# Performance work log

Measured on AMD Instinct MI355X. Metric: run time of the kernel, lower is better.

Reference implementation:

```python
import jax, jax.numpy as jnp
import numpy as np

D = 1024
H = 16
HD = D // H
EPS = 1e-6


def setup_inputs() -> dict:
    key = jax.random.key(0)
    ks = jax.random.split(key, 10)
    s = 1.0 / np.sqrt(D)
    inp = {
        "x": jax.random.normal(ks[0], (2, 2048, D), dtype=jnp.float32),
        "Wq": jax.random.uniform(ks[1], (D, D), jnp.float32, -s, s),
        "bq": jax.random.uniform(ks[2], (D,), jnp.float32, -s, s),
        "Wk": jax.random.uniform(ks[3], (D, D), jnp.float32, -s, s),
        "bk": jax.random.uniform(ks[4], (D,), jnp.float32, -s, s),
        "Wv": jax.random.uniform(ks[5], (D, D), jnp.float32, -s, s),
        "bv": jax.random.uniform(ks[6], (D,), jnp.float32, -s, s),
        "Wo": jax.random.uniform(ks[7], (D, D), jnp.float32, -s, s),
        "bo": jax.random.uniform(ks[8], (D,), jnp.float32, -s, s),
        "gamma": jnp.ones((D,), jnp.float32),
        "beta": jnp.zeros((D,), jnp.float32),
    }
    return inp


def _mha(x, Wq, bq, Wk, bk, Wv, bv, Wo, bo, gamma, beta):
    B, S, _ = x.shape
    # Linear projections (torch Linear: x @ W.T + b), split heads -> [B,H,S,hd]
    q = (x @ Wq.T + bq).reshape(B, S, H, HD).transpose(0, 2, 1, 3)
    k = (x @ Wk.T + bk).reshape(B, S, H, HD).transpose(0, 2, 1, 3)
    v = (x @ Wv.T + bv).reshape(B, S, H, HD).transpose(0, 2, 1, 3)
    scores = jnp.einsum("bhqd,bhkd->bhqk", q, k) / jnp.sqrt(jnp.float32(HD))
    attn = jax.nn.softmax(scores, axis=-1)
    ctx = jnp.einsum("bhqk,bhkd->bhqd", attn, v)
    ctx = ctx.transpose(0, 2, 1, 3).reshape(B, S, D)
    out = ctx @ Wo.T + bo  # dropout p=0.0 -> identity
    res = x + out
    mu = jnp.mean(res, axis=-1, keepdims=True)
    var = jnp.mean(jnp.square(res - mu), axis=-1, keepdims=True)
    return (res - mu) / jnp.sqrt(var + EPS) * gamma + beta


def reference(x, Wq, bq, Wk, bk, Wv, bv, Wo, bo, gamma, beta):
    return _mha(x, Wq, bq, Wk, bk, Wv, bv, Wo, bo, gamma, beta)
```

## Files before the change

kernel.cpp:

```cpp
#include <hip/hip_runtime.h>
#include <hip/hip_bf16.h>
#include <math.h>

#define D_MODEL 1024
#define NH 16
#define HDIM 64
#define BB 2
#define SS 2048
#define MTOK (BB*SS)

typedef __hip_bfloat16 bf16;
typedef short s8v __attribute__((ext_vector_type(8)));
typedef float f4v __attribute__((ext_vector_type(4)));
typedef float f16v __attribute__((ext_vector_type(16)));

__device__ __forceinline__ float bf2f(bf16 x) { return __bfloat162float(x); }
__device__ __forceinline__ bf16 f2bf(float x) { return __float2bfloat16(x); }

typedef const __attribute__((address_space(1))) unsigned int* gas_u32;
typedef __attribute__((address_space(3))) unsigned int* las_u32;
#define ASYNC16(gp, lp) __builtin_amdgcn_global_load_lds((gas_u32)(gp), (las_u32)(lp), 16, 0, 0)

#define QSCALE 0.18033688f

__device__ __forceinline__ unsigned int pack_bf16(float a, float b) {
    unsigned int ua = __builtin_bit_cast(unsigned int, a);
    unsigned int ub = __builtin_bit_cast(unsigned int, b);
    return ((ua + 0x8000u) >> 16) | ((ub + 0x8000u) & 0xffff0000u);
}

__global__ __launch_bounds__(256)
void cvt_kernel(const float* __restrict__ x,  const float* __restrict__ wq,
                const float* __restrict__ wk, const float* __restrict__ wv,
                const float* __restrict__ wo, bf16* __restrict__ dst)
{
    const size_t e = ((size_t)blockIdx.x * 256 + threadIdx.x) * 4;
    const size_t M1 = (size_t)1 << 20;
    const float* src; size_t off;
    if      (e < 4 * M1) { src = x;  off = e;          }
    else if (e < 5 * M1) { src = wq; off = e - 4 * M1; }
    else if (e < 6 * M1) { src = wk; off = e - 5 * M1; }
    else if (e < 7 * M1) { src = wv; off = e - 6 * M1; }
    else                 { src = wo; off = e - 7 * M1; }
    const float4 v = *(const float4*)&src[off];
    bf16 h[4] = { f2bf(v.x), f2bf(v.y), f2bf(v.z), f2bf(v.w) };
    *(uint2*)&dst[e] = *(const uint2*)h;
}

__global__ __launch_bounds__(256, 2)
void gemm_qkv(const bf16* __restrict__ X,
              const bf16* __restrict__ Wq, const float* __restrict__ bq,
              const bf16* __restrict__ Wk, const float* __restrict__ bk,
              const bf16* __restrict__ Wv, const float* __restrict__ bv,
              bf16* __restrict__ q_ws, bf16* __restrict__ k_ws, bf16* __restrict__ v_ws)
{
    const int mat = blockIdx.z;
    const bf16*  W    = (mat == 0) ? Wq : ((mat == 1) ? Wk : Wv);
    const float* bias = (mat == 0) ? bq : ((mat == 1) ? bk : bv);

    const int t = threadIdx.x;
    const int lane = t & 63, wave = t >> 6;
    const int wrow = wave >> 1, wcol = wave & 1;
    const int quad = lane >> 4, l15 = lane & 15;

    const bf16 *Ap, *Bp; int m0, n0;
    if (mat < 2) { Ap = X; Bp = W; m0 = blockIdx.y * 128; n0 = blockIdx.x * 128; }
    else         { Ap = W; Bp = X; m0 = blockIdx.x * 128; n0 = blockIdx.y * 128; }

    __shared__ __align__(16) bf16 As[128 * 64];
    __shared__ __align__(16) bf16 Bs[128 * 64];

    f4v acc[4][4];
#pragma unroll
    for (int i = 0; i < 4; i++)
#pragma unroll
        for (int j = 0; j < 4; j++) acc[i][j] = (f4v){0.f, 0.f, 0.f, 0.f};

    for (int kk = 0; kk < D_MODEL; kk += 64) {
#pragma unroll
        for (int p = 0; p < 4; p++) {
            const int c = p * 256 + t;
            const int row = c >> 3, j = c & 7;
            ASYNC16(&Ap[(size_t)(m0 + row) * D_MODEL + kk + (j ^ (row & 7)) * 8], &As[c * 8]);
        }
#pragma unroll
        for (int p = 0; p < 4; p++) {
            const int c = p * 256 + t;
            const int row = c >> 3, j = c & 7;
            ASYNC16(&Bp[(size_t)(n0 + row) * D_MODEL + kk + (j ^ (row & 7)) * 8], &Bs[c * 8]);
        }
        __syncthreads();

#pragma unroll
        for (int ks = 0; ks < 2; ks++) {
            s8v af[4], bf_[4];
#pragma unroll
            for (int i = 0; i < 4; i++) {
                const int row = wrow * 64 + i * 16 + l15;
                const int g = (ks * 4 + quad) ^ (row & 7);
                af[i] = *(const s8v*)&As[row * 64 + g * 8];
            }
#pragma unroll
            for (int j = 0; j < 4; j++) {
                const int row = wcol * 64 + j * 16 + l15;
                const int g = (ks * 4 + quad) ^ (row & 7);
                bf_[j] = *(const s8v*)&Bs[row * 64 + g * 8];
            }
#pragma unroll
            for (int i = 0; i < 4; i++)
#pragma unroll
                for (int j = 0; j < 4; j++)
                    acc[i][j] = __builtin_amdgcn_mfma_f32_16x16x32_bf16(af[i], bf_[j], acc[i][j], 0, 0, 0);
        }
        __syncthreads();
    }

    if (mat == 2) {
#pragma unroll
        for (int i = 0; i < 4; i++) {
#pragma unroll
            for (int r = 0; r < 4; r++) {
                const int f = m0 + wrow * 64 + i * 16 + quad * 4 + r;
                const float bv_ = bias[f];
#pragma unroll
                for (int j = 0; j < 4; j++) {
                    const int tok = n0 + wcol * 64 + j * 16 + l15;
                    const int b = tok >> 11, s = tok & 2047;
                    v_ws[((size_t)(b * D_MODEL + f)) * SS + s] = f2bf(acc[i][j][r] + bv_);
                }
            }
        }
    } else {
        bf16* dst = (mat == 0) ? q_ws : k_ws;
        const float scale = (mat == 0) ? QSCALE : 1.0f;
#pragma unroll
        for (int j = 0; j < 4; j++) {
            const int col = n0 + wcol * 64 + j * 16 + l15;
            const float bv_ = bias[col];
            const int h = col >> 6, hd = col & 63;
#pragma unroll
            for (int i = 0; i < 4; i++) {
#pragma unroll
                for (int r = 0; r < 4; r++) {
                    const int row = m0 + wrow * 64 + i * 16 + quad * 4 + r;
                    const int b = row >> 11, s = row & 2047;
                    const float v = (acc[i][j][r] + bv_) * scale;
                    dst[(((size_t)(b * NH + h)) * SS + s) * HDIM + hd] = f2bf(v);
                }
            }
        }
    }
}

__global__ __launch_bounds__(256, 2)
void attn_kernel(const bf16* __restrict__ Q, const bf16* __restrict__ K,
                 const bf16* __restrict__ VtG, bf16* __restrict__ ctx)
{
    const int s_ = blockIdx.x;
    const int lb = (s_ & 7) * 64 + (s_ >> 3);
    const int bh = lb >> 4;
    const int q0 = (lb & 15) * 128;
    const bf16* Qp = Q   + (size_t)bh * SS * HDIM;
    const bf16* Kp = K   + (size_t)bh * SS * HDIM;
    const bf16* Vp = VtG + (size_t)bh * HDIM * SS;

    __shared__ __align__(16) bf16 Qs[128 * 64];
    __shared__ __align__(16) bf16 Ks[2][128 * 64];
    __shared__ __align__(16) bf16 Vt[2][64 * 128];

    const int t = threadIdx.x;
    const int lane = t & 63, wave = t >> 6;
    const int l31 = lane & 31, L5 = lane >> 5;
    const int qb = wave * 32;

    const int vrbase = t >> 4;
    const int vcol = (t & 15) * 8;
    uint4 vv[4];
#pragma unroll
    for (int p = 0; p < 4; p++)
        vv[p] = *(const uint4*)&Vp[(size_t)(p * 16 + vrbase) * SS + vcol];
#pragma unroll
    for (int p = 0; p < 4; p++) {
        const int c = p * 256 + t;
        const int row = c >> 3, j = c & 7;
        ASYNC16(&Kp[(size_t)row * HDIM + (j ^ (row & 7)) * 8], &Ks[0][c * 8]);
    }
#pragma unroll
    for (int p = 0; p < 4; p++) {
        const int c = p * 256 + t;
        const int row = c >> 3, g = (c & 7) ^ (row & 7);
        *(uint4*)&Qs[row * 64 + g * 8] = *(const uint4*)&Qp[(size_t)(q0 + row) * HDIM + (c & 7) * 8];
    }
    const int cA = vcol,     pA = (cA & ~12) | ((cA & 4) << 1) | ((cA & 8) >> 1);
    const int cB = vcol + 4, pB = (cB & ~12) | ((cB & 4) << 1) | ((cB & 8) >> 1);
    {
        union { uint4 u4; uint2 u2[2]; } uu;
#pragma unroll
        for (int p = 0; p < 4; p++) {
            const int vr = p * 16 + vrbase;
            uu.u4 = vv[p];
            *(uint2*)&Vt[0][vr * 128 + (((pA >> 3) ^ (vr & 15)) * 8) + (pA & 7)] = uu.u2[0];
            *(uint2*)&Vt[0][vr * 128 + (((pB >> 3) ^ (vr & 15)) * 8) + (pB & 7)] = uu.u2[1];
        }
    }
    __syncthreads();

    s8v qf[4];
#pragma unroll
    for (int kc = 0; kc < 4; kc++) {
        const int g = (kc * 2 + L5) ^ (l31 & 7);
        qf[kc] = *(const s8v*)&Qs[(qb + l31) * 64 + g * 8];
    }

    float l_own = 0.f;
    f16v o_acc[2];
#pragma unroll
    for (int i = 0; i < 16; i++) { o_acc[0][i] = 0.f; o_acc[1][i] = 0.f; }

    int cur = 0;
    for (int it = 0; it < SS / 128; ++it) {
        const bool have = (it < SS / 128 - 1);
        const int s0n = (it + 1) * 128;

        uint4 nv0, nv1, nv2, nv3;
        if (have) {
            nv0 = *(const uint4*)&Vp[(size_t)(0 * 16 + vrbase) * SS + s0n + vcol];
            nv1 = *(const uint4*)&Vp[(size_t)(1 * 16 + vrbase) * SS + s0n + vcol];
            nv2 = *(const uint4*)&Vp[(size_t)(2 * 16 + vrbase) * SS + s0n + vcol];
            nv3 = *(const uint4*)&Vp[(size_t)(3 * 16 + vrbase) * SS + s0n + vcol];
#pragma unroll
            for (int p = 0; p < 4; p++) {
                const int c = p * 256 + t;
                const int row = c >> 3, j = c & 7;
                ASYNC16(&Kp[(size_t)(s0n + row) * HDIM + (j ^ (row & 7)) * 8],
                        &Ks[cur ^ 1][c * 8]);
            }
        }

        const bf16* Ksc = &Ks[cur][0];
        const bf16* Vtc = &Vt[cur][0];
#pragma unroll
        for (int mt = 0; mt < 4; mt++) {
            f16v sc;
#pragma unroll
            for (int i = 0; i < 16; i++) sc[i] = 0.f;
            __builtin_amdgcn_s_setprio(1);
#pragma unroll
            for (int kc = 0; kc < 4; kc++) {
                const int g = (kc * 2 + L5) ^ (l31 & 7);
                const s8v kf = *(const s8v*)&Ksc[(mt * 32 + l31) * 64 + g * 8];
                sc = __builtin_amdgcn_mfma_f32_32x32x16_bf16(kf, qf[kc], sc, 0, 0, 0);
            }
            __builtin_amdgcn_s_setprio(0);
            float tps = 0.f;
#pragma unroll
            for (int i = 0; i < 16; i++) { sc[i] = __builtin_amdgcn_exp2f(sc[i]); tps += sc[i]; }
            l_own += tps;
            unsigned int pk[8];
#pragma unroll
            for (int i = 0; i < 8; i++) pk[i] = pack_bf16(sc[2 * i], sc[2 * i + 1]);
            __builtin_amdgcn_s_setprio(1);
#pragma unroll
            for (int c = 0; c < 2; c++) {
                const s8v pf = *(const s8v*)&pk[c * 4];
#pragma unroll
                for (int dt = 0; dt < 2; dt++) {
                    const int g = (mt * 4 + c * 2 + L5) ^ (l31 & 15);
                    const s8v vf = *(const s8v*)&Vtc[(dt * 32 + l31) * 128 + g * 8];
                    o_acc[dt] = __builtin_amdgcn_mfma_f32_32x32x16_bf16(pf, vf, o_acc[dt], 0, 0, 0);
                }
            }
            __builtin_amdgcn_s_setprio(0);
        }

        if (have) {
            bf16* VtN = &Vt[cur ^ 1][0];
            union { uint4 u4; uint2 u2[2]; } uu;
            const int vr0 = 0 * 16 + vrbase, vr1 = 1 * 16 + vrbase;
            const int vr2 = 2 * 16 + vrbase, vr3 = 3 * 16 + vrbase;
            uu.u4 = nv0;
            *(uint2*)&VtN[vr0 * 128 + (((pA >> 3) ^ (vr0 & 15)) * 8) + (pA & 7)] = uu.u2[0];
            *(uint2*)&VtN[vr0 * 128 + (((pB >> 3) ^ (vr0 & 15)) * 8) + (pB & 7)] = uu.u2[1];
            uu.u4 = nv1;
            *(uint2*)&VtN[vr1 * 128 + (((pA >> 3) ^ (vr1 & 15)) * 8) + (pA & 7)] = uu.u2[0];
            *(uint2*)&VtN[vr1 * 128 + (((pB >> 3) ^ (vr1 & 15)) * 8) + (pB & 7)] = uu.u2[1];
            uu.u4 = nv2;
            *(uint2*)&VtN[vr2 * 128 + (((pA >> 3) ^ (vr2 & 15)) * 8) + (pA & 7)] = uu.u2[0];
            *(uint2*)&VtN[vr2 * 128 + (((pB >> 3) ^ (vr2 & 15)) * 8) + (pB & 7)] = uu.u2[1];
            uu.u4 = nv3;
            *(uint2*)&VtN[vr3 * 128 + (((pA >> 3) ^ (vr3 & 15)) * 8) + (pA & 7)] = uu.u2[0];
            *(uint2*)&VtN[vr3 * 128 + (((pB >> 3) ^ (vr3 & 15)) * 8) + (pB & 7)] = uu.u2[1];
        }
        __syncthreads();
        cur ^= 1;
    }

    const float l_full = l_own + __shfl_xor(l_own, 32);
    const float linv = 1.0f / l_full;
    const int b = bh >> 4, h = bh & 15;
#pragma unroll
    for (int reg = 0; reg < 16; reg++) {
        const int R = (reg & 3) + 8 * (reg >> 2) + 4 * L5;
        const float lr = __shfl(linv, R);
        const int tok = q0 + qb + R;
        const size_t rb = ((size_t)(b * SS + tok)) * D_MODEL + h * 64;
        ctx[rb + l31]      = f2bf(o_acc[0][reg] * lr);
        ctx[rb + 32 + l31] = f2bf(o_acc[1][reg] * lr);
    }
}

__global__ __launch_bounds__(256, 2)
void gemm_oproj(const bf16* __restrict__ Ctx, const bf16* __restrict__ Wo,
                const float* __restrict__ bo, const float* __restrict__ X,
                float* __restrict__ res)
{
    const int m0 = blockIdx.y * 128, n0 = blockIdx.x * 128;
    const int t = threadIdx.x;
    const int lane = t & 63, wave = t >> 6;
    const int wrow = wave >> 1, wcol = wave & 1;
    const int quad = lane >> 4, l15 = lane & 15;

    __shared__ __align__(16) bf16 As[128 * 64];
    __shared__ __align__(16) bf16 Bs[128 * 64];

    f4v acc[4][4];
#pragma unroll
    for (int i = 0; i < 4; i++)
#pragma unroll
        for (int j = 0; j < 4; j++) acc[i][j] = (f4v){0.f, 0.f, 0.f, 0.f};

    for (int kk = 0; kk < D_MODEL; kk += 64) {
#pragma unroll
        for (int p = 0; p < 4; p++) {
            const int c = p * 256 + t;
            const int row = c >> 3, j = c & 7;
            ASYNC16(&Ctx[(size_t)(m0 + row) * D_MODEL + kk + (j ^ (row & 7)) * 8], &As[c * 8]);
        }
#pragma unroll
        for (int p = 0; p < 4; p++) {
            const int c = p * 256 + t;
            const int row = c >> 3, j = c & 7;
            ASYNC16(&Wo[(size_t)(n0 + row) * D_MODEL + kk + (j ^ (row & 7)) * 8], &Bs[c * 8]);
        }
        __syncthreads();

#pragma unroll
        for (int ks = 0; ks < 2; ks++) {
            s8v af[4], bf_[4];
#pragma unroll
            for (int i = 0; i < 4; i++) {
                const int row = wrow * 64 + i * 16 + l15;
                const int g = (ks * 4 + quad) ^ (row & 7);
                af[i] = *(const s8v*)&As[row * 64 + g * 8];
            }
#pragma unroll
            for (int j = 0; j < 4; j++) {
                const int row = wcol * 64 + j * 16 + l15;
                const int g = (ks * 4 + quad) ^ (row & 7);
                bf_[j] = *(const s8v*)&Bs[row * 64 + g * 8];
            }
#pragma unroll
            for (int i = 0; i < 4; i++)
#pragma unroll
                for (int j = 0; j < 4; j++)
                    acc[i][j] = __builtin_amdgcn_mfma_f32_16x16x32_bf16(af[i], bf_[j], acc[i][j], 0, 0, 0);
        }
        __syncthreads();
    }

#pragma unroll
    for (int j = 0; j < 4; j++) {
        const int col = n0 + wcol * 64 + j * 16 + l15;
        const float bv_ = bo[col];
#pragma unroll
        for (int i = 0; i < 4; i++) {
#pragma unroll
            for (int r = 0; r < 4; r++) {
                const int row = m0 + wrow * 64 + i * 16 + quad * 4 + r;
                const size_t idx = (size_t)row * D_MODEL + col;
                res[idx] = acc[i][j][r] + bv_ + X[idx];
            }
        }
    }
}

__global__ __launch_bounds__(256)
void ln_kernel(const float* __restrict__ res, const float* __restrict__ gamma,
               const float* __restrict__ beta, float* __restrict__ out)
{
    const int row = blockIdx.x;
    const int t = threadIdx.x;
    const float4 v = *(const float4*)&res[(size_t)row * D_MODEL + t * 4];

    float s = v.x + v.y + v.z + v.w;
    float sq = v.x * v.x + v.y * v.y + v.z * v.z + v.w * v.w;
#pragma unroll
    for (int m = 1; m < 64; m <<= 1) {
        s += __shfl_xor(s, m);
        sq += __shfl_xor(sq, m);
    }
    __shared__ float red[8];
    const int wave = t >> 6, lane = t & 63;
    if (lane == 0) { red[wave] = s; red[4 + wave] = sq; }
    __syncthreads();
    s = red[0] + red[1] + red[2] + red[3];
    sq = red[4] + red[5] + red[6] + red[7];
    const float mu = s * (1.0f / D_MODEL);
    const float var = sq * (1.0f / D_MODEL) - mu * mu;
    const float rstd = rsqrtf(var + 1e-6f);

    const float vv[4] = {v.x, v.y, v.z, v.w};
    float4 o;
    o.x = (vv[0] - mu) * rstd * gamma[t * 4 + 0] + beta[t * 4 + 0];
    o.y = (vv[1] - mu) * rstd * gamma[t * 4 + 1] + beta[t * 4 + 1];
    o.z = (vv[2] - mu) * rstd * gamma[t * 4 + 2] + beta[t * 4 + 2];
    o.w = (vv[3] - mu) * rstd * gamma[t * 4 + 3] + beta[t * 4 + 3];
    *(float4*)&out[(size_t)row * D_MODEL + t * 4] = o;
}

extern "C" void kernel_launch(void* const* d_in, const int* in_sizes, int n_in,
                              void* d_out, int out_size, void* d_ws, size_t ws_size,
                              hipStream_t stream) {
    const float* x     = (const float*)d_in[0];
    const float* Wq    = (const float*)d_in[1];
    const float* bq    = (const float*)d_in[2];
    const float* Wk    = (const float*)d_in[3];
    const float* bk    = (const float*)d_in[4];
    const float* Wv    = (const float*)d_in[5];
    const float* bv    = (const float*)d_in[6];
    const float* Wo    = (const float*)d_in[7];
    const float* bo    = (const float*)d_in[8];
    const float* gamma = (const float*)d_in[9];
    const float* beta  = (const float*)d_in[10];
    float* out = (float*)d_out;

    char* ws = (char*)d_ws;
    bf16* xb  = (bf16*)(ws);
    bf16* Wqb = (bf16*)(ws + ((size_t)8 << 20));
    bf16* Wkb = (bf16*)(ws + ((size_t)10 << 20));
    bf16* Wvb = (bf16*)(ws + ((size_t)12 << 20));
    bf16* Wob = (bf16*)(ws + ((size_t)14 << 20));
    bf16*  q_ws   = (bf16*)(ws + ((size_t)16 << 20));
    bf16*  k_ws   = (bf16*)(ws + ((size_t)24 << 20));
    bf16*  v_ws   = (bf16*)(ws + ((size_t)32 << 20));
    bf16*  ctx_ws = (bf16*)(ws + ((size_t)40 << 20));
    float* res_ws = (float*)(ws + ((size_t)16 << 20));

    cvt_kernel<<<8192, 256, 0, stream>>>(x, Wq, Wk, Wv, Wo, xb);
    gemm_qkv<<<dim3(8, 32, 3), 256, 0, stream>>>(xb, Wqb, bq, Wkb, bk, Wvb, bv, q_ws, k_ws, v_ws);
    attn_kernel<<<512, 256, 0, stream>>>(q_ws, k_ws, v_ws, ctx_ws);
    gemm_oproj<<<dim3(8, 32), 256, 0, stream>>>(ctx_ws, Wob, bo, x, res_ws);
    ln_kernel<<<MTOK, 256, 0, stream>>>(res_ws, gamma, beta, out);
}
```

Before: 209.0 us.

## Double-buffer GEMM LDS tiles, software-pipeline QK MFMA, use hardware bf16 pack

The QKV and output-projection GEMMs now use two LDS buffers per operand, prefetching the next K-slice asynchronously while the current one is consumed, which removes one barrier per iteration. In attention, the QK^T MFMA tile for the next 32-key slice is issued before the exp/PV work of the current slice, so matrix and vector work can overlap. The manual round-to-nearest bf16 packing is replaced by the v_cvt_pk_bf16_f32 instruction. The cost is doubled LDS in the GEMMs (which may lower occupancy) and more live registers in attention. The loop issues no wait on the prefetched loads before the barrier, so whether the next buffer is complete when read depends on how the compiler places vmcnt waits.

```diff
diff --git a/kernel.cpp b/kernel.cpp
--- a/kernel.cpp
+++ b/kernel.cpp
@@ -23,10 +23,10 @@
 
 #define QSCALE 0.18033688f
 
-__device__ __forceinline__ unsigned int pack_bf16(float a, float b) {
-    unsigned int ua = __builtin_bit_cast(unsigned int, a);
-    unsigned int ub = __builtin_bit_cast(unsigned int, b);
-    return ((ua + 0x8000u) >> 16) | ((ub + 0x8000u) & 0xffff0000u);
+__device__ __forceinline__ unsigned int cvtpk_bf16(float a, float b) {
+    unsigned int r;
+    asm("v_cvt_pk_bf16_f32 %0, %1, %2" : "=v"(r) : "v"(a), "v"(b));
+    return r;
 }
 
 __global__ __launch_bounds__(256)
@@ -67,8 +67,8 @@
     if (mat < 2) { Ap = X; Bp = W; m0 = blockIdx.y * 128; n0 = blockIdx.x * 128; }
     else         { Ap = W; Bp = X; m0 = blockIdx.x * 128; n0 = blockIdx.y * 128; }
 
-    __shared__ __align__(16) bf16 As[128 * 64];
-    __shared__ __align__(16) bf16 Bs[128 * 64];
+    __shared__ __align__(16) bf16 As[2][128 * 64];
+    __shared__ __align__(16) bf16 Bs[2][128 * 64];
 
     f4v acc[4][4];
 #pragma unroll
@@ -76,20 +76,26 @@
 #pragma unroll
         for (int j = 0; j < 4; j++) acc[i][j] = (f4v){0.f, 0.f, 0.f, 0.f};
 
+#pragma unroll
+    for (int p = 0; p < 4; p++) {
+        const int c = p * 256 + t;
+        const int row = c >> 3, j = c & 7;
+        ASYNC16(&Ap[(size_t)(m0 + row) * D_MODEL + (j ^ (row & 7)) * 8], &As[0][c * 8]);
+        ASYNC16(&Bp[(size_t)(n0 + row) * D_MODEL + (j ^ (row & 7)) * 8], &Bs[0][c * 8]);
+    }
+    __syncthreads();
+
+    int cur = 0;
     for (int kk = 0; kk < D_MODEL; kk += 64) {
-#pragma unroll
-        for (int p = 0; p < 4; p++) {
-            const int c = p * 256 + t;
-            const int row = c >> 3, j = c & 7;
-            ASYNC16(&Ap[(size_t)(m0 + row) * D_MODEL + kk + (j ^ (row & 7)) * 8], &As[c * 8]);
-        }
-#pragma unroll
-        for (int p = 0; p < 4; p++) {
-            const int c = p * 256 + t;
-            const int row = c >> 3, j = c & 7;
-            ASYNC16(&Bp[(size_t)(n0 + row) * D_MODEL + kk + (j ^ (row & 7)) * 8], &Bs[c * 8]);
-        }
-        __syncthreads();
+        if (kk + 64 < D_MODEL) {
+#pragma unroll
+            for (int p = 0; p < 4; p++) {
+                const int c = p * 256 + t;
+                const int row = c >> 3, j = c & 7;
+                ASYNC16(&Ap[(size_t)(m0 + row) * D_MODEL + kk + 64 + (j ^ (row & 7)) * 8], &As[cur ^ 1][c * 8]);
+                ASYNC16(&Bp[(size_t)(n0 + row) * D_MODEL + kk + 64 + (j ^ (row & 7)) * 8], &Bs[cur ^ 1][c * 8]);
+            }
+        }
 
 #pragma unroll
         for (int ks = 0; ks < 2; ks++) {
@@ -98,13 +104,13 @@
             for (int i = 0; i < 4; i++) {
                 const int row = wrow * 64 + i * 16 + l15;
                 const int g = (ks * 4 + quad) ^ (row & 7);
-                af[i] = *(const s8v*)&As[row * 64 + g * 8];
+                af[i] = *(const s8v*)&As[cur][row * 64 + g * 8];
             }
 #pragma unroll
             for (int j = 0; j < 4; j++) {
                 const int row = wcol * 64 + j * 16 + l15;
                 const int g = (ks * 4 + quad) ^ (row & 7);
-                bf_[j] = *(const s8v*)&Bs[row * 64 + g * 8];
+                bf_[j] = *(const s8v*)&Bs[cur][row * 64 + g * 8];
             }
 #pragma unroll
             for (int i = 0; i < 4; i++)
@@ -112,7 +118,8 @@
                 for (int j = 0; j < 4; j++)
                     acc[i][j] = __builtin_amdgcn_mfma_f32_16x16x32_bf16(af[i], bf_[j], acc[i][j], 0, 0, 0);
         }
-        __syncthreads();
+        if (kk + 64 < D_MODEL) __syncthreads();
+        cur ^= 1;
     }
 
     if (mat == 2) {
@@ -150,6 +157,23 @@
             }
         }
     }
+}
+
+__device__ __forceinline__ f16v qk_tile(const bf16* Ksc, const s8v* qf,
+                                        const int mt, const int l31, const int L5)
+{
+    f16v sc;
+#pragma unroll
+    for (int i = 0; i < 16; i++) sc[i] = 0.f;
+    __builtin_amdgcn_s_setprio(1);
+#pragma unroll
+    for (int kc = 0; kc < 4; kc++) {
+        const int g = (kc * 2 + L5) ^ (l31 & 7);
+        const s8v kf = *(const s8v*)&Ksc[(mt * 32 + l31) * 64 + g * 8];
+        sc = __builtin_amdgcn_mfma_f32_32x32x16_bf16(kf, qf[kc], sc, 0, 0, 0);
+    }
+    __builtin_amdgcn_s_setprio(0);
+    return sc;
 }
 
 __global__ __launch_bounds__(256, 2)
@@ -239,26 +263,19 @@
 
         const bf16* Ksc = &Ks[cur][0];
         const bf16* Vtc = &Vt[cur][0];
+
+        f16v sc_cur = qk_tile(Ksc, qf, 0, l31, L5);
 #pragma unroll
         for (int mt = 0; mt < 4; mt++) {
-            f16v sc;
-#pragma unroll
-            for (int i = 0; i < 16; i++) sc[i] = 0.f;
-            __builtin_amdgcn_s_setprio(1);
-#pragma unroll
-            for (int kc = 0; kc < 4; kc++) {
-                const int g = (kc * 2 + L5) ^ (l31 & 7);
-                const s8v kf = *(const s8v*)&Ksc[(mt * 32 + l31) * 64 + g * 8];
-                sc = __builtin_amdgcn_mfma_f32_32x32x16_bf16(kf, qf[kc], sc, 0, 0, 0);
-            }
-            __builtin_amdgcn_s_setprio(0);
+            f16v sc_nxt;
+            if (mt < 3) sc_nxt = qk_tile(Ksc, qf, mt + 1, l31, L5);
             float tps = 0.f;
 #pragma unroll
-            for (int i = 0; i < 16; i++) { sc[i] = __builtin_amdgcn_exp2f(sc[i]); tps += sc[i]; }
+            for (int i = 0; i < 16; i++) { sc_cur[i] = __builtin_amdgcn_exp2f(sc_cur[i]); tps += sc_cur[i]; }
             l_own += tps;
             unsigned int pk[8];
 #pragma unroll
-            for (int i = 0; i < 8; i++) pk[i] = pack_bf16(sc[2 * i], sc[2 * i + 1]);
+            for (int i = 0; i < 8; i++) pk[i] = cvtpk_bf16(sc_cur[2 * i], sc_cur[2 * i + 1]);
             __builtin_amdgcn_s_setprio(1);
 #pragma unroll
             for (int c = 0; c < 2; c++) {
@@ -271,6 +288,7 @@
                 }
             }
             __builtin_amdgcn_s_setprio(0);
+            sc_cur = sc_nxt;
         }
 
         if (have) {
@@ -320,8 +338,8 @@
     const int wrow = wave >> 1, wcol = wave & 1;
     const int quad = lane >> 4, l15 = lane & 15;
 
-    __shared__ __align__(16) bf16 As[128 * 64];
-    __shared__ __align__(16) bf16 Bs[128 * 64];
+    __shared__ __align__(16) bf16 As[2][128 * 64];
+    __shared__ __align__(16) bf16 Bs[2][128 * 64];
 
     f4v acc[4][4];
 #pragma unroll
@@ -329,20 +347,26 @@
 #pragma unroll
         for (int j = 0; j < 4; j++) acc[i][j] = (f4v){0.f, 0.f, 0.f, 0.f};
 
+#pragma unroll
+    for (int p = 0; p < 4; p++) {
+        const int c = p * 256 + t;
+        const int row = c >> 3, j = c & 7;
+        ASYNC16(&Ctx[(size_t)(m0 + row) * D_MODEL + (j ^ (row & 7)) * 8], &As[0][c * 8]);
+        ASYNC16(&Wo[(size_t)(n0 + row) * D_MODEL + (j ^ (row & 7)) * 8],  &Bs[0][c * 8]);
+    }
+    __syncthreads();
+
+    int cur = 0;
     for (int kk = 0; kk < D_MODEL; kk += 64) {
-#pragma unroll
-        for (int p = 0; p < 4; p++) {
-            const int c = p * 256 + t;
-            const int row = c >> 3, j = c & 7;
-            ASYNC16(&Ctx[(size_t)(m0 + row) * D_MODEL + kk + (j ^ (row & 7)) * 8], &As[c * 8]);
-        }
-#pragma unroll
-        for (int p = 0; p < 4; p++) {
-            const int c = p * 256 + t;
-            const int row = c >> 3, j = c & 7;
-            ASYNC16(&Wo[(size_t)(n0 + row) * D_MODEL + kk + (j ^ (row & 7)) * 8], &Bs[c * 8]);
-        }
-        __syncthreads();
+        if (kk + 64 < D_MODEL) {
+#pragma unroll
+            for (int p = 0; p < 4; p++) {
+                const int c = p * 256 + t;
+                const int row = c >> 3, j = c & 7;
+                ASYNC16(&Ctx[(size_t)(m0 + row) * D_MODEL + kk + 64 + (j ^ (row & 7)) * 8], &As[cur ^ 1][c * 8]);
+                ASYNC16(&Wo[(size_t)(n0 + row) * D_MODEL + kk + 64 + (j ^ (row & 7)) * 8],  &Bs[cur ^ 1][c * 8]);
+            }
+        }
 
 #pragma unroll
         for (int ks = 0; ks < 2; ks++) {
@@ -351,13 +375,13 @@
             for (int i = 0; i < 4; i++) {
                 const int row = wrow * 64 + i * 16 + l15;
                 const int g = (ks * 4 + quad) ^ (row & 7);
-                af[i] = *(const s8v*)&As[row * 64 + g * 8];
+                af[i] = *(const s8v*)&As[cur][row * 64 + g * 8];
             }
 #pragma unroll
             for (int j = 0; j < 4; j++) {
                 const int row = wcol * 64 + j * 16 + l15;
                 const int g = (ks * 4 + quad) ^ (row & 7);
-                bf_[j] = *(const s8v*)&Bs[row * 64 + g * 8];
+                bf_[j] = *(const s8v*)&Bs[cur][row * 64 + g * 8];
             }
 #pragma unroll
             for (int i = 0; i < 4; i++)
@@ -365,7 +389,8 @@
                 for (int j = 0; j < 4; j++)
                     acc[i][j] = __builtin_amdgcn_mfma_f32_16x16x32_bf16(af[i], bf_[j], acc[i][j], 0, 0, 0);
         }
-        __syncthreads();
+        if (kk + 64 < D_MODEL) __syncthreads();
+        cur ^= 1;
     }
 
 #pragma unroll
```

Result: slower. 215.5 us (+3.1%).

## Split attention key tiles across two wave groups with 512-thread blocks

Applied to the files above, without the earlier changes.

The attention kernel now runs 512 threads per block. Waves 4-7 handle the second half of each 128-key tile for the same query rows, and at the end the two halves' partial outputs and row sums are combined through shared memory. This doubles the waves available to hide latency per block and halves the tile loads each thread issues. The cost is a final reduction through LDS and possibly lower occupancy given the launch-bounds change. The manual bf16 pack is also replaced with the hardware v_cvt_pk_bf16_f32 instruction.

```diff
diff --git a/kernel.cpp b/kernel.cpp
--- a/kernel.cpp
+++ b/kernel.cpp
@@ -23,10 +23,10 @@
 
 #define QSCALE 0.18033688f
 
-__device__ __forceinline__ unsigned int pack_bf16(float a, float b) {
-    unsigned int ua = __builtin_bit_cast(unsigned int, a);
-    unsigned int ub = __builtin_bit_cast(unsigned int, b);
-    return ((ua + 0x8000u) >> 16) | ((ub + 0x8000u) & 0xffff0000u);
+__device__ __forceinline__ unsigned int cvtpk_bf16(float a, float b) {
+    unsigned int r;
+    asm("v_cvt_pk_bf16_f32 %0, %1, %2" : "=v"(r) : "v"(a), "v"(b));
+    return r;
 }
 
 __global__ __launch_bounds__(256)
@@ -152,7 +152,24 @@
     }
 }
 
-__global__ __launch_bounds__(256, 2)
+__device__ __forceinline__ f16v qk_tile(const bf16* Ksc, const s8v* qf,
+                                        const int mt, const int l31, const int L5)
+{
+    f16v sc;
+#pragma unroll
+    for (int i = 0; i < 16; i++) sc[i] = 0.f;
+    __builtin_amdgcn_s_setprio(1);
+#pragma unroll
+    for (int kc = 0; kc < 4; kc++) {
+        const int g = (kc * 2 + L5) ^ (l31 & 7);
+        const s8v kf = *(const s8v*)&Ksc[(mt * 32 + l31) * 64 + g * 8];
+        sc = __builtin_amdgcn_mfma_f32_32x32x16_bf16(kf, qf[kc], sc, 0, 0, 0);
+    }
+    __builtin_amdgcn_s_setprio(0);
+    return sc;
+}
+
+__global__ __launch_bounds__(512, 4)
 void attn_kernel(const bf16* __restrict__ Q, const bf16* __restrict__ K,
                  const bf16* __restrict__ VtG, bf16* __restrict__ ctx)
 {
@@ -171,23 +188,24 @@
     const int t = threadIdx.x;
     const int lane = t & 63, wave = t >> 6;
     const int l31 = lane & 31, L5 = lane >> 5;
-    const int qb = wave * 32;
+    const int qb = (wave & 3) * 32;
+    const int half = wave >> 2;
 
     const int vrbase = t >> 4;
     const int vcol = (t & 15) * 8;
-    uint4 vv[4];
-#pragma unroll
-    for (int p = 0; p < 4; p++)
-        vv[p] = *(const uint4*)&Vp[(size_t)(p * 16 + vrbase) * SS + vcol];
-#pragma unroll
-    for (int p = 0; p < 4; p++) {
-        const int c = p * 256 + t;
+    uint4 vv[2];
+#pragma unroll
+    for (int p = 0; p < 2; p++)
+        vv[p] = *(const uint4*)&Vp[(size_t)(p * 32 + vrbase) * SS + vcol];
+#pragma unroll
+    for (int p = 0; p < 2; p++) {
+        const int c = p * 512 + t;
         const int row = c >> 3, j = c & 7;
         ASYNC16(&Kp[(size_t)row * HDIM + (j ^ (row & 7)) * 8], &Ks[0][c * 8]);
     }
 #pragma unroll
-    for (int p = 0; p < 4; p++) {
-        const int c = p * 256 + t;
+    for (int p = 0; p < 2; p++) {
+        const int c = p * 512 + t;
         const int row = c >> 3, g = (c & 7) ^ (row & 7);
         *(uint4*)&Qs[row * 64 + g * 8] = *(const uint4*)&Qp[(size_t)(q0 + row) * HDIM + (c & 7) * 8];
     }
@@ -196,8 +214,8 @@
     {
         union { uint4 u4; uint2 u2[2]; } uu;
 #pragma unroll
-        for (int p = 0; p < 4; p++) {
-            const int vr = p * 16 + vrbase;
+        for (int p = 0; p < 2; p++) {
+            const int vr = p * 32 + vrbase;
             uu.u4 = vv[p];
             *(uint2*)&Vt[0][vr * 128 + (((pA >> 3) ^ (vr & 15)) * 8) + (pA & 7)] = uu.u2[0];
             *(uint2*)&Vt[0][vr * 128 + (((pB >> 3) ^ (vr & 15)) * 8) + (pB & 7)] = uu.u2[1];
@@ -222,15 +240,13 @@
         const bool have = (it < SS / 128 - 1);
         const int s0n = (it + 1) * 128;
 
-        uint4 nv0, nv1, nv2, nv3;
+        uint4 nv0, nv1;
         if (have) {
-            nv0 = *(const uint4*)&Vp[(size_t)(0 * 16 + vrbase) * SS + s0n + vcol];
-            nv1 = *(const uint4*)&Vp[(size_t)(1 * 16 + vrbase) * SS + s0n + vcol];
-            nv2 = *(const uint4*)&Vp[(size_t)(2 * 16 + vrbase) * SS + s0n + vcol];
-            nv3 = *(const uint4*)&Vp[(size_t)(3 * 16 + vrbase) * SS + s0n + vcol];
-#pragma unroll
-            for (int p = 0; p < 4; p++) {
-                const int c = p * 256 + t;
+            nv0 = *(const uint4*)&Vp[(size_t)(vrbase) * SS + s0n + vcol];
+            nv1 = *(const uint4*)&Vp[(size_t)(32 + vrbase) * SS + s0n + vcol];
+#pragma unroll
+            for (int p = 0; p < 2; p++) {
+                const int c = p * 512 + t;
                 const int row = c >> 3, j = c & 7;
                 ASYNC16(&Kp[(size_t)(s0n + row) * HDIM + (j ^ (row & 7)) * 8],
                         &Ks[cur ^ 1][c * 8]);
@@ -240,25 +256,16 @@
         const bf16* Ksc = &Ks[cur][0];
         const bf16* Vtc = &Vt[cur][0];
 #pragma unroll
-        for (int mt = 0; mt < 4; mt++) {
-            f16v sc;
-#pragma unroll
-            for (int i = 0; i < 16; i++) sc[i] = 0.f;
-            __builtin_amdgcn_s_setprio(1);
-#pragma unroll
-            for (int kc = 0; kc < 4; kc++) {
-                const int g = (kc * 2 + L5) ^ (l31 & 7);
-                const s8v kf = *(const s8v*)&Ksc[(mt * 32 + l31) * 64 + g * 8];
-                sc = __builtin_amdgcn_mfma_f32_32x32x16_bf16(kf, qf[kc], sc, 0, 0, 0);
-            }
-            __builtin_amdgcn_s_setprio(0);
+        for (int mt2 = 0; mt2 < 2; mt2++) {
+            const int mt = half * 2 + mt2;
+            f16v sc = qk_tile(Ksc, qf, mt, l31, L5);
             float tps = 0.f;
 #pragma unroll
             for (int i = 0; i < 16; i++) { sc[i] = __builtin_amdgcn_exp2f(sc[i]); tps += sc[i]; }
             l_own += tps;
             unsigned int pk[8];
 #pragma unroll
-            for (int i = 0; i < 8; i++) pk[i] = pack_bf16(sc[2 * i], sc[2 * i + 1]);
+            for (int i = 0; i < 8; i++) pk[i] = cvtpk_bf16(sc[2 * i], sc[2 * i + 1]);
             __builtin_amdgcn_s_setprio(1);
 #pragma unroll
             for (int c = 0; c < 2; c++) {
@@ -276,36 +283,47 @@
         if (have) {
             bf16* VtN = &Vt[cur ^ 1][0];
             union { uint4 u4; uint2 u2[2]; } uu;
-            const int vr0 = 0 * 16 + vrbase, vr1 = 1 * 16 + vrbase;
-            const int vr2 = 2 * 16 + vrbase, vr3 = 3 * 16 + vrbase;
+            const int vr0 = vrbase, vr1 = 32 + vrbase;
             uu.u4 = nv0;
             *(uint2*)&VtN[vr0 * 128 + (((pA >> 3) ^ (vr0 & 15)) * 8) + (pA & 7)] = uu.u2[0];
             *(uint2*)&VtN[vr0 * 128 + (((pB >> 3) ^ (vr0 & 15)) * 8) + (pB & 7)] = uu.u2[1];
             uu.u4 = nv1;
             *(uint2*)&VtN[vr1 * 128 + (((pA >> 3) ^ (vr1 & 15)) * 8) + (pA & 7)] = uu.u2[0];
             *(uint2*)&VtN[vr1 * 128 + (((pB >> 3) ^ (vr1 & 15)) * 8) + (pB & 7)] = uu.u2[1];
-            uu.u4 = nv2;
-            *(uint2*)&VtN[vr2 * 128 + (((pA >> 3) ^ (vr2 & 15)) * 8) + (pA & 7)] = uu.u2[0];
-            *(uint2*)&VtN[vr2 * 128 + (((pB >> 3) ^ (vr2 & 15)) * 8) + (pB & 7)] = uu.u2[1];
-            uu.u4 = nv3;
-            *(uint2*)&VtN[vr3 * 128 + (((pA >> 3) ^ (vr3 & 15)) * 8) + (pA & 7)] = uu.u2[0];
-            *(uint2*)&VtN[vr3 * 128 + (((pB >> 3) ^ (vr3 & 15)) * 8) + (pB & 7)] = uu.u2[1];
         }
         __syncthreads();
         cur ^= 1;
     }
 
-    const float l_full = l_own + __shfl_xor(l_own, 32);
-    const float linv = 1.0f / l_full;
-    const int b = bh >> 4, h = bh & 15;
-#pragma unroll
-    for (int reg = 0; reg < 16; reg++) {
-        const int R = (reg & 3) + 8 * (reg >> 2) + 4 * L5;
-        const float lr = __shfl(linv, R);
-        const int tok = q0 + qb + R;
-        const size_t rb = ((size_t)(b * SS + tok)) * D_MODEL + h * 64;
-        ctx[rb + l31]      = f2bf(o_acc[0][reg] * lr);
-        ctx[rb + 32 + l31] = f2bf(o_acc[1][reg] * lr);
+    const float l_wave = l_own + __shfl_xor(l_own, 32);
+    float* o_sh = (float*)&Ks[0][0];
+    float* l_sh = (float*)&Vt[0][0];
+    if (half == 1) {
+        const int pr = wave & 3;
+#pragma unroll
+        for (int dt = 0; dt < 2; dt++)
+#pragma unroll
+            for (int reg = 0; reg < 16; reg++)
+                o_sh[((pr * 2 + dt) * 16 + reg) * 64 + lane] = o_acc[dt][reg];
+        if (lane < 32) l_sh[pr * 32 + l31] = l_wave;
+    }
+    __syncthreads();
+    if (half == 0) {
+        const int pr = wave;
+        const float linv = 1.0f / (l_wave + l_sh[pr * 32 + l31]);
+        const int b = bh >> 4, h = bh & 15;
+#pragma unroll
+        for (int reg = 0; reg < 16; reg++) {
+            const int R = (reg & 3) + 8 * (reg >> 2) + 4 * L5;
+            const float lr = __shfl(linv, R);
+            const int tok = q0 + qb + R;
+            const size_t rb = ((size_t)(b * SS + tok)) * D_MODEL + h * 64;
+#pragma unroll
+            for (int dt = 0; dt < 2; dt++) {
+                const float val = o_acc[dt][reg] + o_sh[((pr * 2 + dt) * 16 + reg) * 64 + lane];
+                ctx[rb + dt * 32 + l31] = f2bf(val * lr);
+            }
+        }
     }
 }
 
@@ -448,7 +466,7 @@
 
     cvt_kernel<<<8192, 256, 0, stream>>>(x, Wq, Wk, Wv, Wo, xb);
     gemm_qkv<<<dim3(8, 32, 3), 256, 0, stream>>>(xb, Wqb, bq, Wkb, bk, Wvb, bv, q_ws, k_ws, v_ws);
-    attn_kernel<<<512, 256, 0, stream>>>(q_ws, k_ws, v_ws, ctx_ws);
+    attn_kernel<<<512, 512, 0, stream>>>(q_ws, k_ws, v_ws, ctx_ws);
     gemm_oproj<<<dim3(8, 32), 256, 0, stream>>>(ctx_ws, Wob, bo, x, res_ws);
     ln_kernel<<<MTOK, 256, 0, stream>>>(res_ws, gamma, beta, out);
 }
```

Result: faster. 200.1 us (-4.3%).
